# Performance work log

Hardware: AMD Instinct MI355X
Metric: run time of the kernel (lower is better)

Reference implementation:

```python
import jax, jax.numpy as jnp
import numpy as np

B, S, CC, CF, E, H, NH = 16, 1024, 8, 8, 64, 1024, 16
DH = H // NH
VOCAB = 10000
EPS = 1e-5


def layer_norm(x, g, b):
    m = x.mean(-1, keepdims=True)
    v = x.var(-1, keepdims=True)
    return (x - m) / jnp.sqrt(v + EPS) * g + b


def setup_inputs():
    key = jax.random.key(0)
    ks = jax.random.split(key, 30)
    f32 = jnp.float32
    n = lambda k, shp, s=0.02: jax.random.normal(k, shp, f32) * s
    inp = {}
    inp['cate_x'] = jax.random.randint(ks[0], (B, S, CC), 0, VOCAB)
    inp['cont_x'] = jax.random.normal(ks[1], (B, S, CF), f32)
    inp['mask'] = jax.random.randint(ks[2], (B, S), 0, 2)
    # parameters
    inp['emb_table'] = n(ks[3], (VOCAB, E)).at[0].set(0.0)  # padding_idx=0
    inp['cate_W'] = n(ks[4], (CC * E, H)); inp['cate_b'] = jnp.zeros((H,), f32)
    inp['cate_ln_g'] = jnp.ones((H,), f32); inp['cate_ln_b'] = jnp.zeros((H,), f32)
    inp['bn_g'] = jnp.ones((CF,), f32); inp['bn_b'] = jnp.zeros((CF,), f32)
    inp['cont_W'] = n(ks[5], (CF, H)); inp['cont_b'] = jnp.zeros((H,), f32)
    inp['cont_ln_g'] = jnp.ones((H,), f32); inp['cont_ln_b'] = jnp.zeros((H,), f32)
    inp['comb_W'] = n(ks[6], (2 * H, H)); inp['comb_b'] = jnp.zeros((H,), f32)
    inp['comb_ln_g'] = jnp.ones((H,), f32); inp['comb_ln_b'] = jnp.zeros((H,), f32)
    inp['Wq'] = n(ks[7], (H, H)); inp['bq'] = jnp.zeros((H,), f32)
    inp['Wk'] = n(ks[8], (H, H)); inp['bk'] = jnp.zeros((H,), f32)
    inp['Wv'] = n(ks[9], (H, H)); inp['bv'] = jnp.zeros((H,), f32)
    inp['Wo'] = n(ks[10], (H, H)); inp['bo'] = jnp.zeros((H,), f32)
    return inp


def reference(cate_x, cont_x, mask, emb_table, cate_W, cate_b, cate_ln_g, cate_ln_b,
              bn_g, bn_b, cont_W, cont_b, cont_ln_g, cont_ln_b,
              comb_W, comb_b, comb_ln_g, comb_ln_b,
              Wq, bq, Wk, bk, Wv, bv, Wo, bo):
    # categorical path: embed -> flatten cols -> Linear+LN
    cate_emb = emb_table[cate_x].reshape(B, S, CC * E)
    cate_h = layer_norm(cate_emb @ cate_W + cate_b, cate_ln_g, cate_ln_b)
    # continuous path: BatchNorm1d over flattened (B*S, CF) with batch stats
    xf = cont_x.reshape(-1, CF)
    mu = xf.mean(0)
    var = xf.var(0)  # biased, as torch BN normalization
    xn = ((xf - mu) / jnp.sqrt(var + EPS) * bn_g + bn_b).reshape(B, S, CF)
    cont_h = layer_norm(xn @ cont_W + cont_b, cont_ln_g, cont_ln_b)
    # combine: ReLU -> Linear -> LN
    seq = jax.nn.relu(jnp.concatenate([cate_h, cont_h], axis=2))
    x = layer_norm(seq @ comb_W + comb_b, comb_ln_g, comb_ln_b)  # [B,S,H]
    # multi-head attention (dropout is identity in eval)
    Q = (x @ Wq + bq).reshape(B, S, NH, DH)
    K = (x @ Wk + bk).reshape(B, S, NH, DH)
    V = (x @ Wv + bv).reshape(B, S, NH, DH)
    scores = jnp.einsum('bqhd,bkhd->bhqk', Q, K) / np.sqrt(DH).astype(np.float32)
    # faithful to source: mask broadcast over the QUERY axis
    scores = jnp.where(mask[:, None, :, None] == 0, -1e7, scores)
    attn = jax.nn.softmax(scores, axis=-1)
    out = jnp.einsum('bhqk,bkhd->bqhd', attn, V).reshape(B, S, H)
    out = out @ Wo + bo
    return out[:, -1:, -1]  # [B,1]
```

## Files before the change

### kernel.cpp

```cpp
#include <hip/hip_runtime.h>
#include <hip/hip_bf16.h>
#include <math.h>

#define EPS 1e-5f

typedef unsigned short u16;
typedef __attribute__((ext_vector_type(8))) short bf16x8;
typedef __attribute__((ext_vector_type(4))) float f32x4;

__device__ __forceinline__ float b2f(u16 u) {
  union { unsigned int i; float f; } v; v.i = ((unsigned int)u) << 16; return v.f;
}
__device__ __forceinline__ u16 f2b(float f) {
  union { float f; unsigned int i; } v; v.f = f;
  unsigned int r = v.i + 0x7fff + ((v.i >> 16) & 1);
  return (u16)(r >> 16);
}

__device__ __forceinline__ void gload_lds16(const u16* g, u16* l) {
  __builtin_amdgcn_global_load_lds(
      (const __attribute__((address_space(1))) unsigned int*)g,
      (__attribute__((address_space(3))) unsigned int*)l, 16, 0, 0);
}

__global__ __launch_bounds__(256) void prep_k(
    const float* __restrict__ cx, float* __restrict__ part_bn,
    float* __restrict__ outacc,
    const float* __restrict__ emb, u16* __restrict__ embb,
    const float* __restrict__ cate_W, u16* __restrict__ cateWT,
    const float* __restrict__ comb_W, u16* __restrict__ combWT,
    const float* __restrict__ Wv, const float* __restrict__ Wo,
    float* __restrict__ wvo) {
  __shared__ float shmem[64 * 65];
  const int bid = blockIdx.x, tid = threadIdx.x;

  if (bid == 0) {
    if (tid < 16) outacc[tid] = 0.f;
    return;
  }
  if (bid <= 64) {
    int pb = bid - 1;
    int gid = pb * 256 + tid;
    float4 a = ((const float4*)cx)[2 * gid];
    float4 b = ((const float4*)cx)[2 * gid + 1];
    float v[16];
    v[0] = a.x; v[1] = a.y; v[2] = a.z; v[3] = a.w;
    v[4] = b.x; v[5] = b.y; v[6] = b.z; v[7] = b.w;
#pragma unroll
    for (int i = 0; i < 8; ++i) v[8 + i] = v[i] * v[i];
#pragma unroll
    for (int off = 32; off; off >>= 1)
#pragma unroll
      for (int i = 0; i < 16; ++i) v[i] += __shfl_down(v[i], off);
    int l = tid & 63, wv_ = tid >> 6;
    if (l == 0)
#pragma unroll
      for (int i = 0; i < 16; ++i) shmem[wv_ * 16 + i] = v[i];
    __syncthreads();
    if (tid < 16)
      part_bn[pb * 16 + tid] = shmem[tid] + shmem[16 + tid] + shmem[32 + tid] + shmem[48 + tid];
    return;
  }
  if (bid <= 689) {
    int i = (bid - 65) * 256 + tid;
    if (i < 160000) {
      float4 v = ((const float4*)emb)[i];
      ushort4 u; u.x = f2b(v.x); u.y = f2b(v.y); u.z = f2b(v.z); u.w = f2b(v.w);
      ((ushort4*)embb)[i] = u;
    }
    return;
  }
  if (bid <= 1329) {
    const float* W; u16* WT; int K, local;
    if (bid <= 817) { W = cate_W; WT = cateWT; K = 512;  local = bid - 690; }
    else            { W = comb_W; WT = combWT; K = 2048; local = bid - 818; }
    int n0 = (local & 15) * 64, k0 = (local >> 4) * 64;
    int c = tid & 63, r0 = tid >> 6;
#pragma unroll
    for (int i = 0; i < 16; ++i) {
      int r = r0 + i * 4;
      shmem[r * 65 + c] = W[(size_t)(k0 + r) * 1024 + n0 + c];
    }
    __syncthreads();
#pragma unroll
    for (int i = 0; i < 16; ++i) {
      int r = r0 + i * 4;
      WT[(size_t)(n0 + r) * K + k0 + c] = f2b(shmem[c * 65 + r]);
    }
    return;
  }
  {
    int local = bid - 1330;
    int h = local >> 2, jc = local & 3;
    if (tid < 64) shmem[tid] = Wo[(size_t)(h * 64 + tid) * 1024 + 1023];
    __syncthreads();
    int j = jc * 256 + tid;
    const float* vr = Wv + (size_t)j * 1024 + h * 64;
    float s = 0.f;
    for (int d4 = 0; d4 < 64; d4 += 4) {
      float4 w4 = *(const float4*)(vr + d4);
      s = fmaf(w4.x, shmem[d4], s);
      s = fmaf(w4.y, shmem[d4 + 1], s);
      s = fmaf(w4.z, shmem[d4 + 2], s);
      s = fmaf(w4.w, shmem[d4 + 3], s);
    }
    wvo[h * 1024 + j] = s;
  }
}

template <int MODE, int VC>
__global__ __launch_bounds__(512) void gemm256(
    const u16* __restrict__ A0, const u16* __restrict__ A1,
    const int* __restrict__ idx, const u16* __restrict__ embb,
    const u16* __restrict__ BT, const float* __restrict__ bias,
    u16* __restrict__ C, int K) {
  __shared__ u16 As[2][2][8192];
  __shared__ u16 Bs[2][2][8192];
  const int tid = threadIdx.x;
  const int bid = blockIdx.x;
  const int chunk = gridDim.x >> 3;
  const int swz = (bid & 7) * chunk + (bid >> 3);
  const int row0 = (swz >> 2) * 256;
  const int col0 = (swz & 3) * 256;

  const int rr8 = tid >> 3;
  const int p8  = tid & 7;
  const int sl  = p8 ^ (rr8 & 7);

  const int l   = tid & 63;
  const int w   = tid >> 6;
  const int wrh = w >> 2;
  const int wcq = w & 3;
  const int hb  = wcq >> 1;
  const int rbb = (wcq & 1) * 64;
  const int lr  = l & 15;
  const int lk  = l >> 4;

  f32x4 acc[8][4];
#pragma unroll
  for (int m = 0; m < 8; ++m)
#pragma unroll
    for (int n = 0; n < 4; ++n) acc[m][n] = (f32x4){0.f, 0.f, 0.f, 0.f};

  const int nt = K >> 6;

  auto stage = [&](int t, int buf) {
    const int k0 = t << 6;
#pragma unroll
    for (int h = 0; h < 2; ++h)
#pragma unroll
      for (int i = 0; i < 2; ++i) {
        int ar = row0 + h * 128 + i * 64 + rr8;
        const u16* asrc;
        if (MODE == 1) {
          int id = idx[ar * 8 + (k0 >> 6)];
          asrc = embb + (size_t)id * 64 + sl * 8;
        } else {
          const u16* base = (k0 < 1024) ? A0 : A1;
          asrc = base + (size_t)ar * 1024 + (k0 & 1023) + sl * 8;
        }
        gload_lds16(asrc, &As[buf][h][i * 4096 + tid * 8]);
      }
#pragma unroll
    for (int h = 0; h < 2; ++h)
#pragma unroll
      for (int i = 0; i < 2; ++i) {
        int br = col0 + h * 128 + i * 64 + rr8;
        gload_lds16(BT + (size_t)br * K + k0 + sl * 8,
                    &Bs[buf][h][i * 4096 + tid * 8]);
      }
  };

  stage(0, 0);

  for (int t = 0; t < nt; ++t) {
    if (t + 1 < nt) {
      stage(t + 1, (t + 1) & 1);
      if (VC == 8) asm volatile("s_waitcnt vmcnt(8)" ::: "memory");
      else         asm volatile("s_waitcnt vmcnt(12)" ::: "memory");
    } else {
      asm volatile("s_waitcnt vmcnt(0)" ::: "memory");
    }
    __builtin_amdgcn_s_barrier();

    const int cur = t & 1;

    auto loadA = [&](bf16x8 (&af)[2][2], int q) {
#pragma unroll
      for (int mm = 0; mm < 2; ++mm)
#pragma unroll
        for (int ks = 0; ks < 2; ++ks) {
          int rowa = (q * 2 + mm) * 16 + lr;
          int ph = (ks * 4 + lk) ^ (lr & 7);
          af[mm][ks] = *(const bf16x8*)&As[cur][wrh][rowa * 64 + ph * 8];
        }
    };

    bf16x8 bfr[4][2];
#pragma unroll
    for (int n = 0; n < 4; ++n)
#pragma unroll
      for (int ks = 0; ks < 2; ++ks) {
        int rowb = rbb + n * 16 + lr;
        int ph = (ks * 4 + lk) ^ (lr & 7);
        bfr[n][ks] = *(const bf16x8*)&Bs[cur][hb][rowb * 64 + ph * 8];
      }

    auto mfma_quad = [&](bf16x8 (&af)[2][2], int q) {
      __builtin_amdgcn_s_setprio(1);
#pragma unroll
      for (int ks = 0; ks < 2; ++ks)
#pragma unroll
        for (int mm = 0; mm < 2; ++mm)
#pragma unroll
          for (int n = 0; n < 4; ++n)
            acc[q * 2 + mm][n] = __builtin_amdgcn_mfma_f32_16x16x32_bf16(
                af[mm][ks], bfr[n][ks], acc[q * 2 + mm][n], 0, 0, 0);
      __builtin_amdgcn_s_setprio(0);
    };

    bf16x8 afr0[2][2], afr1[2][2];
    loadA(afr0, 0);
    loadA(afr1, 1);
    mfma_quad(afr0, 0);
    loadA(afr0, 2);
    mfma_quad(afr1, 1);
    loadA(afr1, 3);
    mfma_quad(afr0, 2);
    mfma_quad(afr1, 3);

    if (t + 1 < nt) __builtin_amdgcn_s_barrier();
  }

  float bv_[4];
#pragma unroll
  for (int n = 0; n < 4; ++n) bv_[n] = bias[col0 + wcq * 64 + n * 16 + lr];
#pragma unroll
  for (int m = 0; m < 8; ++m) {
#pragma unroll
    for (int n = 0; n < 4; ++n) {
      int cc = col0 + wcq * 64 + n * 16 + lr;
#pragma unroll
      for (int q4 = 0; q4 < 4; ++q4) {
        int rr = row0 + wrh * 128 + m * 16 + lk * 4 + q4;
        C[(size_t)rr * 1024 + cc] = f2b(acc[m][n][q4] + bv_[n]);
      }
    }
  }
}

__global__ __launch_bounds__(256) void ln_k(u16* __restrict__ buf,
                                            const float* __restrict__ g,
                                            const float* __restrict__ b, int relu) {
  int lane = threadIdx.x & 63, wave = threadIdx.x >> 6;
  size_t row = (size_t)blockIdx.x * 4 + wave;
  u16* p = buf + row * 1024 + lane * 16;
  uint4 u0 = *(uint4*)p;
  uint4 u1 = *(uint4*)(p + 8);
  float x[16];
#pragma unroll
  for (int i = 0; i < 4; ++i) {
    unsigned int w0 = ((unsigned int*)&u0)[i];
    unsigned int w1 = ((unsigned int*)&u1)[i];
    x[2 * i]     = b2f((u16)(w0 & 0xffff));
    x[2 * i + 1] = b2f((u16)(w0 >> 16));
    x[8 + 2 * i]     = b2f((u16)(w1 & 0xffff));
    x[8 + 2 * i + 1] = b2f((u16)(w1 >> 16));
  }
  float s = 0.f, s2 = 0.f;
#pragma unroll
  for (int i = 0; i < 16; ++i) { s += x[i]; s2 += x[i] * x[i]; }
#pragma unroll
  for (int off = 32; off; off >>= 1) { s += __shfl_xor(s, off); s2 += __shfl_xor(s2, off); }
  float mean = s * (1.f / 1024.f);
  float var = s2 * (1.f / 1024.f) - mean * mean;
  float rs = rsqrtf(var + EPS);
  float y[16];
#pragma unroll
  for (int q = 0; q < 4; ++q) {
    float4 gv = *(const float4*)(g + lane * 16 + q * 4);
    float4 bv = *(const float4*)(b + lane * 16 + q * 4);
    y[4 * q]     = (x[4 * q]     - mean) * rs * gv.x + bv.x;
    y[4 * q + 1] = (x[4 * q + 1] - mean) * rs * gv.y + bv.y;
    y[4 * q + 2] = (x[4 * q + 2] - mean) * rs * gv.z + bv.z;
    y[4 * q + 3] = (x[4 * q + 3] - mean) * rs * gv.w + bv.w;
  }
  if (relu)
#pragma unroll
    for (int i = 0; i < 16; ++i) y[i] = fmaxf(y[i], 0.f);
  uint4 o0, o1;
#pragma unroll
  for (int i = 0; i < 4; ++i) {
    ((unsigned int*)&o0)[i] = (unsigned int)f2b(y[2 * i]) | ((unsigned int)f2b(y[2 * i + 1]) << 16);
    ((unsigned int*)&o1)[i] = (unsigned int)f2b(y[8 + 2 * i]) | ((unsigned int)f2b(y[8 + 2 * i + 1]) << 16);
  }
  *(uint4*)p = o0;
  *(uint4*)(p + 8) = o1;
}

__global__ __launch_bounds__(256) void cont_k(const float* __restrict__ cx,
                                              const float* __restrict__ part_bn,
                                              const float* __restrict__ bn_g,
                                              const float* __restrict__ bn_b,
                                              const float* __restrict__ W,
                                              const float* __restrict__ cb,
                                              const float* __restrict__ g,
                                              const float* __restrict__ bb,
                                              u16* __restrict__ out) {
  int row0 = blockIdx.x * 8, tid = threadIdx.x;
  __shared__ float sp[4][16];
  __shared__ float tt[16];
  __shared__ float ab[2][8];
  __shared__ float xn[8][8];
  __shared__ float rr1[4][8], rr2[4][8];

  if (tid < 64) {
    int f = tid & 15, qd = tid >> 4;
    float s = 0.f;
    for (int j = qd * 16; j < qd * 16 + 16; ++j) s += part_bn[j * 16 + f];
    sp[qd][f] = s;
  }
  __syncthreads();
  if (tid < 16) tt[tid] = sp[0][tid] + sp[1][tid] + sp[2][tid] + sp[3][tid];
  __syncthreads();
  if (tid < 8) {
    float mu = tt[tid] * (1.f / 16384.f);
    float var = tt[8 + tid] * (1.f / 16384.f) - mu * mu;
    float a = rsqrtf(var + EPS) * bn_g[tid];
    ab[0][tid] = a;
    ab[1][tid] = bn_b[tid] - mu * a;
  }
  __syncthreads();
  if (tid < 64) {
    int r = tid >> 3, f = tid & 7;
    xn[r][f] = ab[0][f] * cx[(row0 + r) * 8 + f] + ab[1][f];
  }
  __syncthreads();

  int c = tid * 4;
  float4 cbv = *(const float4*)(cb + c);
  float acc[8][4];
#pragma unroll
  for (int r = 0; r < 8; ++r) {
    acc[r][0] = cbv.x; acc[r][1] = cbv.y; acc[r][2] = cbv.z; acc[r][3] = cbv.w;
  }
  for (int k = 0; k < 8; ++k) {
    float4 w4 = *(const float4*)(W + k * 1024 + c);
#pragma unroll
    for (int r = 0; r < 8; ++r) {
      float xv = xn[r][k];
      acc[r][0] = fmaf(xv, w4.x, acc[r][0]);
      acc[r][1] = fmaf(xv, w4.y, acc[r][1]);
      acc[r][2] = fmaf(xv, w4.z, acc[r][2]);
      acc[r][3] = fmaf(xv, w4.w, acc[r][3]);
    }
  }
  float s1[8], s2[8];
#pragma unroll
  for (int r = 0; r < 8; ++r) {
    s1[r] = acc[r][0] + acc[r][1] + acc[r][2] + acc[r][3];
    s2[r] = acc[r][0] * acc[r][0] + acc[r][1] * acc[r][1] +
            acc[r][2] * acc[r][2] + acc[r][3] * acc[r][3];
  }
#pragma unroll
  for (int off = 32; off; off >>= 1)
#pragma unroll
    for (int r = 0; r < 8; ++r) {
      s1[r] += __shfl_down(s1[r], off);
      s2[r] += __shfl_down(s2[r], off);
    }
  int lane = tid & 63, wv = tid >> 6;
  if (lane == 0)
#pragma unroll
    for (int r = 0; r < 8; ++r) { rr1[wv][r] = s1[r]; rr2[wv][r] = s2[r]; }
  __syncthreads();
  float4 gv = *(const float4*)(g + c);
  float4 bv = *(const float4*)(bb + c);
#pragma unroll
  for (int r = 0; r < 8; ++r) {
    float ss = rr1[0][r] + rr1[1][r] + rr1[2][r] + rr1[3][r];
    float qq = rr2[0][r] + rr2[1][r] + rr2[2][r] + rr2[3][r];
    float mean = ss * (1.f / 1024.f);
    float var = qq * (1.f / 1024.f) - mean * mean;
    float rs = rsqrtf(var + EPS);
    float y0 = fmaxf((acc[r][0] - mean) * rs * gv.x + bv.x, 0.f);
    float y1 = fmaxf((acc[r][1] - mean) * rs * gv.y + bv.y, 0.f);
    float y2 = fmaxf((acc[r][2] - mean) * rs * gv.z + bv.z, 0.f);
    float y3 = fmaxf((acc[r][3] - mean) * rs * gv.w + bv.w, 0.f);
    ushort4 o; o.x = f2b(y0); o.y = f2b(y1); o.z = f2b(y2); o.w = f2b(y3);
    *(ushort4*)(out + (size_t)(row0 + r) * 1024 + c) = o;
  }
}

__global__ __launch_bounds__(256) void qproj_k(const u16* __restrict__ x,
                                               const float* __restrict__ Wq,
                                               const float* __restrict__ bq,
                                               float* __restrict__ q) {
  __shared__ u16 xs[16][1024];
  __shared__ float part[16][16][16];
  int tid = threadIdx.x;
  for (int i = tid; i < 4096; i += 256) {
    int b = i >> 8, off = (i & 255) * 4;
    *(ushort4*)&xs[b][off] =
        *(const ushort4*)(x + ((size_t)(b * 1024 + 1023)) * 1024 + off);
  }
  __syncthreads();
  int c = tid & 15;
  int col = blockIdx.x * 16 + c;
  int kq = tid >> 4;
  float acc[16];
#pragma unroll
  for (int b = 0; b < 16; ++b) acc[b] = 0.f;
  for (int k = kq * 64; k < kq * 64 + 64; ++k) {
    float wv = Wq[(size_t)k * 1024 + col];
#pragma unroll
    for (int b = 0; b < 16; ++b) acc[b] = fmaf(b2f(xs[b][k]), wv, acc[b]);
  }
#pragma unroll
  for (int b = 0; b < 16; ++b) part[kq][b][c] = acc[b];
  __syncthreads();
  if (tid < 256) {
    int b = tid >> 4, cc = tid & 15;
    float s = 0.f;
#pragma unroll
    for (int j = 0; j < 16; ++j) s += part[j][b][cc];
    q[b * 1024 + blockIdx.x * 16 + cc] = s + bq[blockIdx.x * 16 + cc];
  }
}

__global__ __launch_bounds__(256) void kq_k(const float* __restrict__ Wk,
                                            const float* __restrict__ bk,
                                            const float* __restrict__ q,
                                            u16* __restrict__ qtb,
                                            float* __restrict__ bkq) {
  int h = blockIdx.x >> 2, jc = blockIdx.x & 3;
  int tid = threadIdx.x;
  __shared__ float Qs[16][64];
  for (int i = tid; i < 1024; i += 256) {
    int b = i >> 6, d = i & 63;
    Qs[b][d] = q[b * 1024 + h * 64 + d];
  }
  __syncthreads();
  int j = jc * 256 + tid;
  float acc[16];
#pragma unroll
  for (int b = 0; b < 16; ++b) acc[b] = 0.f;
  const float* wr = Wk + (size_t)j * 1024 + h * 64;
  for (int d4 = 0; d4 < 64; d4 += 4) {
    float4 w4 = *(const float4*)(wr + d4);
#pragma unroll
    for (int b = 0; b < 16; ++b) {
      acc[b] = fmaf(w4.x, Qs[b][d4], acc[b]);
      acc[b] = fmaf(w4.y, Qs[b][d4 + 1], acc[b]);
      acc[b] = fmaf(w4.z, Qs[b][d4 + 2], acc[b]);
      acc[b] = fmaf(w4.w, Qs[b][d4 + 3], acc[b]);
    }
  }
#pragma unroll
  for (int b = 0; b < 16; ++b) qtb[((size_t)b * 16 + h) * 1024 + j] = f2b(acc[b]);
  if (jc == 0 && tid < 16) {
    int b = tid;
    float s = 0.f;
    for (int d = 0; d < 64; ++d) s = fmaf(bk[h * 64 + d], Qs[b][d], s);
    bkq[b * 16 + h] = s;
  }
}

__global__ __launch_bounds__(256) void score_k(const u16* __restrict__ x,
                                               const u16* __restrict__ qtb,
                                               const float* __restrict__ bkq,
                                               const int* __restrict__ mask,
                                               float* __restrict__ sc) {
  int b = blockIdx.x >> 4, kc = blockIdx.x & 15;
  int tid = threadIdx.x;
  int l = tid & 63, w = tid >> 6;
  int keybase = kc * 64 + w * 16;
  int lr = l & 15, ls = l >> 4;
  int masked = (mask[b * 1024 + 1023] == 0);

  f32x4 acc = (f32x4){0.f, 0.f, 0.f, 0.f};
  const u16* xb = x + (size_t)b * 1024 * 1024;
  const u16* qb = qtb + (size_t)b * 16 * 1024;
  for (int k0 = 0; k0 < 1024; k0 += 32) {
    bf16x8 bfr = *(const bf16x8*)&qb[(size_t)lr * 1024 + k0 + ls * 8];
    bf16x8 afr = *(const bf16x8*)&xb[(size_t)(keybase + lr) * 1024 + k0 + ls * 8];
    acc = __builtin_amdgcn_mfma_f32_16x16x32_bf16(afr, bfr, acc, 0, 0, 0);
  }
  int h = lr;
  float bq_ = bkq[b * 16 + h];
#pragma unroll
  for (int q = 0; q < 4; ++q) {
    int key = keybase + ls * 4 + q;
    float v = masked ? 0.f : (acc[q] + bq_) * 0.125f;
    sc[((size_t)b * 16 + h) * 1024 + key] = v;
  }
}

__global__ __launch_bounds__(256) void attnw_k(float* __restrict__ sc) {
  int bh = blockIdx.x, tid = threadIdx.x;
  float* row = sc + (size_t)bh * 1024;
  float4 v = ((float4*)row)[tid];
  float m = fmaxf(fmaxf(v.x, v.y), fmaxf(v.z, v.w));
#pragma unroll
  for (int off = 32; off; off >>= 1) m = fmaxf(m, __shfl_down(m, off));
  __shared__ float rm[4], rs_[4];
  int lane = tid & 63, wv = tid >> 6;
  if (lane == 0) rm[wv] = m;
  __syncthreads();
  m = fmaxf(fmaxf(rm[0], rm[1]), fmaxf(rm[2], rm[3]));
  float e0 = expf(v.x - m), e1 = expf(v.y - m), e2 = expf(v.z - m), e3 = expf(v.w - m);
  float s = e0 + e1 + e2 + e3;
#pragma unroll
  for (int off = 32; off; off >>= 1) s += __shfl_down(s, off);
  if (lane == 0) rs_[wv] = s;
  __syncthreads();
  s = rs_[0] + rs_[1] + rs_[2] + rs_[3];
  float inv = 1.f / s;
  float4 o; o.x = e0 * inv; o.y = e1 * inv; o.z = e2 * inv; o.w = e3 * inv;
  ((float4*)row)[tid] = o;
}

__global__ __launch_bounds__(256) void ctx_k(const float* __restrict__ p,
                                             const u16* __restrict__ x,
                                             const float* __restrict__ wvo,
                                             float* __restrict__ outacc) {
  int b = blockIdx.x >> 4, kc = blockIdx.x & 15;
  int tid = threadIdx.x;
  __shared__ float pl[64][16];
  for (int i = tid; i < 1024; i += 256) {
    int kk = i >> 4, hh = i & 15;
    pl[kk][hh] = p[((size_t)b * 16 + hh) * 1024 + kc * 64 + kk];
  }
  __syncthreads();
  float acc[16][4];
#pragma unroll
  for (int h = 0; h < 16; ++h)
#pragma unroll
    for (int j = 0; j < 4; ++j) acc[h][j] = 0.f;
  const u16* xb = x + ((size_t)(b * 1024 + kc * 64)) * 1024 + tid * 4;
  for (int k = 0; k < 64; ++k) {
    ushort4 u = *(const ushort4*)(xb + (size_t)k * 1024);
    float x0 = b2f(u.x), x1 = b2f(u.y), x2 = b2f(u.z), x3 = b2f(u.w);
#pragma unroll
    for (int h4 = 0; h4 < 4; ++h4) {
      float4 pv = *(const float4*)&pl[k][h4 * 4];
      acc[h4 * 4 + 0][0] = fmaf(pv.x, x0, acc[h4 * 4 + 0][0]);
      acc[h4 * 4 + 0][1] = fmaf(pv.x, x1, acc[h4 * 4 + 0][1]);
      acc[h4 * 4 + 0][2] = fmaf(pv.x, x2, acc[h4 * 4 + 0][2]);
      acc[h4 * 4 + 0][3] = fmaf(pv.x, x3, acc[h4 * 4 + 0][3]);
      acc[h4 * 4 + 1][0] = fmaf(pv.y, x0, acc[h4 * 4 + 1][0]);
      acc[h4 * 4 + 1][1] = fmaf(pv.y, x1, acc[h4 * 4 + 1][1]);
      acc[h4 * 4 + 1][2] = fmaf(pv.y, x2, acc[h4 * 4 + 1][2]);
      acc[h4 * 4 + 1][3] = fmaf(pv.y, x3, acc[h4 * 4 + 1][3]);
      acc[h4 * 4 + 2][0] = fmaf(pv.z, x0, acc[h4 * 4 + 2][0]);
      acc[h4 * 4 + 2][1] = fmaf(pv.z, x1, acc[h4 * 4 + 2][1]);
      acc[h4 * 4 + 2][2] = fmaf(pv.z, x2, acc[h4 * 4 + 2][2]);
      acc[h4 * 4 + 2][3] = fmaf(pv.z, x3, acc[h4 * 4 + 2][3]);
      acc[h4 * 4 + 3][0] = fmaf(pv.w, x0, acc[h4 * 4 + 3][0]);
      acc[h4 * 4 + 3][1] = fmaf(pv.w, x1, acc[h4 * 4 + 3][1]);
      acc[h4 * 4 + 3][2] = fmaf(pv.w, x2, acc[h4 * 4 + 3][2]);
      acc[h4 * 4 + 3][3] = fmaf(pv.w, x3, acc[h4 * 4 + 3][3]);
    }
  }
  float s = 0.f;
#pragma unroll
  for (int h = 0; h < 16; ++h) {
    float4 w4 = *(const float4*)&wvo[h * 1024 + tid * 4];
    s += acc[h][0] * w4.x + acc[h][1] * w4.y + acc[h][2] * w4.z + acc[h][3] * w4.w;
  }
#pragma unroll
  for (int off = 32; off; off >>= 1) s += __shfl_down(s, off);
  __shared__ float r[4];
  int lane = tid & 63, wv = tid >> 6;
  if (lane == 0) r[wv] = s;
  __syncthreads();
  if (tid == 0) atomicAdd(&outacc[b], r[0] + r[1] + r[2] + r[3]);
}

__global__ __launch_bounds__(256) void bfinal_k(const float* __restrict__ outacc,
                                                const float* __restrict__ bv,
                                                const float* __restrict__ Wo,
                                                const float* __restrict__ bo,
                                                float* __restrict__ out) {
  int tid = threadIdx.x;
  float s = 0.f;
  for (int i = tid; i < 1024; i += 256) s = fmaf(bv[i], Wo[(size_t)i * 1024 + 1023], s);
#pragma unroll
  for (int off = 32; off; off >>= 1) s += __shfl_down(s, off);
  __shared__ float r[4];
  int lane = tid & 63, wv = tid >> 6;
  if (lane == 0) r[wv] = s;
  __syncthreads();
  float bc = r[0] + r[1] + r[2] + r[3] + bo[1023];
  if (tid < 16) out[tid] = outacc[tid] + bc;
}

extern "C" void kernel_launch(void* const* d_in, const int* in_sizes, int n_in,
                              void* d_out, int out_size, void* d_ws, size_t ws_size,
                              hipStream_t stream) {
  const int*   cate_x  = (const int*)d_in[0];
  const float* cont_x  = (const float*)d_in[1];
  const int*   mask    = (const int*)d_in[2];
  const float* emb     = (const float*)d_in[3];
  const float* cate_W  = (const float*)d_in[4];
  const float* cate_b  = (const float*)d_in[5];
  const float* cate_g  = (const float*)d_in[6];
  const float* cate_bb = (const float*)d_in[7];
  const float* bn_g    = (const float*)d_in[8];
  const float* bn_b    = (const float*)d_in[9];
  const float* cont_W  = (const float*)d_in[10];
  const float* cont_b  = (const float*)d_in[11];
  const float* cont_g  = (const float*)d_in[12];
  const float* cont_bb = (const float*)d_in[13];
  const float* Wq = (const float*)d_in[18]; const float* bq = (const float*)d_in[19];
  const float* Wk = (const float*)d_in[20]; const float* bk = (const float*)d_in[21];
  const float* Wv = (const float*)d_in[22]; const float* bv = (const float*)d_in[23];
  const float* Wo = (const float*)d_in[24]; const float* bo = (const float*)d_in[25];
  const float* comb_W  = (const float*)d_in[14];
  const float* comb_b  = (const float*)d_in[15];
  const float* comb_g  = (const float*)d_in[16];
  const float* comb_bb = (const float*)d_in[17];
  float* out = (float*)d_out;

  char* w = (char*)d_ws;
  float* stats   = (float*)w;
  float* outacc  = stats + 16;
  float* part_bn = (float*)(w + 256);
  float* qbuf    = (float*)(w + 8192);
  u16* embb      = (u16*)(w + 131328);
  u16* cateWT    = (u16*)(w + 1411328);
  u16* combWT    = (u16*)(w + 2459904);
  float* sc      = (float*)(w + 6654208);
  u16*   qtb     = (u16*)(w + 7702784);
  float* wvo     = (float*)(w + 8227072);
  float* bkq     = (float*)(w + 8292608);
  u16* X1        = (u16*)(w + 10848512);
  u16* X2        = X1 + (size_t)16777216;
  u16* xb        = X2 + (size_t)16777216;

  prep_k<<<1394, 256, 0, stream>>>(cont_x, part_bn, outacc, emb, embb,
                                   cate_W, cateWT, comb_W, combWT, Wv, Wo, wvo);

  gemm256<1, 12><<<256, 512, 0, stream>>>(nullptr, nullptr, cate_x, embb, cateWT,
                                          cate_b, X1, 512);
  ln_k<<<4096, 256, 0, stream>>>(X1, cate_g, cate_bb, 1);
  cont_k<<<2048, 256, 0, stream>>>(cont_x, part_bn, bn_g, bn_b, cont_W, cont_b,
                                   cont_g, cont_bb, X2);
  gemm256<2, 8><<<256, 512, 0, stream>>>(X1, X2, nullptr, nullptr, combWT,
                                         comb_b, xb, 2048);
  ln_k<<<4096, 256, 0, stream>>>(xb, comb_g, comb_bb, 0);

  qproj_k<<<64, 256, 0, stream>>>(xb, Wq, bq, qbuf);
  kq_k<<<64, 256, 0, stream>>>(Wk, bk, qbuf, qtb, bkq);
  score_k<<<256, 256, 0, stream>>>(xb, qtb, bkq, mask, sc);
  attnw_k<<<256, 256, 0, stream>>>(sc);
  ctx_k<<<256, 256, 0, stream>>>(sc, xb, wvo, outacc);
  bfinal_k<<<1, 256, 0, stream>>>(outacc, bv, Wo, bo, out);
}
```

Before: 212.5 us.

## Interleave half-tile global-to-LDS staging with MFMA quads in 256x256 GEMM

Restructures the bf16 GEMM main loop into a two-tile unrolled schedule. Global-to-LDS loads for the next A tile and the B tile after it are issued in halves between individual MFMA quads, with extra barriers and lgkmcnt waits around each step. The goal is finer-grained overlap of memory traffic with matrix math, in the style of a ping-pong schedule. In exchange it adds many more barriers per K step, relies on hand-counted vmcnt values, and assumes nt is even.

```diff
diff --git a/kernel.cpp b/kernel.cpp
--- a/kernel.cpp
+++ b/kernel.cpp
@@ -108,7 +108,7 @@
   }
 }
 
-template <int MODE, int VC>
+template <int MODE>
 __global__ __launch_bounds__(512) void gemm256(
     const u16* __restrict__ A0, const u16* __restrict__ A1,
     const int* __restrict__ idx, const u16* __restrict__ embb,
@@ -143,93 +143,135 @@
     for (int n = 0; n < 4; ++n) acc[m][n] = (f32x4){0.f, 0.f, 0.f, 0.f};
 
   const int nt = K >> 6;
-
-  auto stage = [&](int t, int buf) {
+  const int nit = nt >> 1;
+
+  auto stageA = [&](int t, int h) {
     const int k0 = t << 6;
-#pragma unroll
-    for (int h = 0; h < 2; ++h)
-#pragma unroll
-      for (int i = 0; i < 2; ++i) {
-        int ar = row0 + h * 128 + i * 64 + rr8;
-        const u16* asrc;
-        if (MODE == 1) {
-          int id = idx[ar * 8 + (k0 >> 6)];
-          asrc = embb + (size_t)id * 64 + sl * 8;
-        } else {
-          const u16* base = (k0 < 1024) ? A0 : A1;
-          asrc = base + (size_t)ar * 1024 + (k0 & 1023) + sl * 8;
-        }
-        gload_lds16(asrc, &As[buf][h][i * 4096 + tid * 8]);
+    const int buf = t & 1;
+#pragma unroll
+    for (int i = 0; i < 2; ++i) {
+      int ar = row0 + h * 128 + i * 64 + rr8;
+      const u16* asrc;
+      if (MODE == 1) {
+        int id = idx[ar * 8 + (k0 >> 6)];
+        asrc = embb + (size_t)id * 64 + sl * 8;
+      } else {
+        const u16* base = (k0 < 1024) ? A0 : A1;
+        asrc = base + (size_t)ar * 1024 + (k0 & 1023) + sl * 8;
       }
-#pragma unroll
-    for (int h = 0; h < 2; ++h)
-#pragma unroll
-      for (int i = 0; i < 2; ++i) {
-        int br = col0 + h * 128 + i * 64 + rr8;
-        gload_lds16(BT + (size_t)br * K + k0 + sl * 8,
-                    &Bs[buf][h][i * 4096 + tid * 8]);
-      }
+      gload_lds16(asrc, &As[buf][h][i * 4096 + tid * 8]);
+    }
   };
-
-  stage(0, 0);
-
-  for (int t = 0; t < nt; ++t) {
-    if (t + 1 < nt) {
-      stage(t + 1, (t + 1) & 1);
-      if (VC == 8) asm volatile("s_waitcnt vmcnt(8)" ::: "memory");
-      else         asm volatile("s_waitcnt vmcnt(12)" ::: "memory");
-    } else {
-      asm volatile("s_waitcnt vmcnt(0)" ::: "memory");
-    }
-    __builtin_amdgcn_s_barrier();
-
-    const int cur = t & 1;
-
-    auto loadA = [&](bf16x8 (&af)[2][2], int q) {
-#pragma unroll
-      for (int mm = 0; mm < 2; ++mm)
-#pragma unroll
-        for (int ks = 0; ks < 2; ++ks) {
-          int rowa = (q * 2 + mm) * 16 + lr;
-          int ph = (ks * 4 + lk) ^ (lr & 7);
-          af[mm][ks] = *(const bf16x8*)&As[cur][wrh][rowa * 64 + ph * 8];
-        }
-    };
-
-    bf16x8 bfr[4][2];
+  auto stageB = [&](int t, int h) {
+    const int k0 = t << 6;
+    const int buf = t & 1;
+#pragma unroll
+    for (int i = 0; i < 2; ++i) {
+      int br = col0 + h * 128 + i * 64 + rr8;
+      gload_lds16(BT + (size_t)br * K + k0 + sl * 8,
+                  &Bs[buf][h][i * 4096 + tid * 8]);
+    }
+  };
+
+  bf16x8 bfr[4][2];
+  auto loadB = [&](int buf) {
 #pragma unroll
     for (int n = 0; n < 4; ++n)
 #pragma unroll
       for (int ks = 0; ks < 2; ++ks) {
         int rowb = rbb + n * 16 + lr;
         int ph = (ks * 4 + lk) ^ (lr & 7);
-        bfr[n][ks] = *(const bf16x8*)&Bs[cur][hb][rowb * 64 + ph * 8];
+        bfr[n][ks] = *(const bf16x8*)&Bs[buf][hb][rowb * 64 + ph * 8];
       }
-
-    auto mfma_quad = [&](bf16x8 (&af)[2][2], int q) {
-      __builtin_amdgcn_s_setprio(1);
-#pragma unroll
-      for (int ks = 0; ks < 2; ++ks)
-#pragma unroll
-        for (int mm = 0; mm < 2; ++mm)
-#pragma unroll
-          for (int n = 0; n < 4; ++n)
-            acc[q * 2 + mm][n] = __builtin_amdgcn_mfma_f32_16x16x32_bf16(
-                af[mm][ks], bfr[n][ks], acc[q * 2 + mm][n], 0, 0, 0);
-      __builtin_amdgcn_s_setprio(0);
-    };
-
-    bf16x8 afr0[2][2], afr1[2][2];
-    loadA(afr0, 0);
-    loadA(afr1, 1);
-    mfma_quad(afr0, 0);
-    loadA(afr0, 2);
-    mfma_quad(afr1, 1);
-    loadA(afr1, 3);
-    mfma_quad(afr0, 2);
-    mfma_quad(afr1, 3);
-
-    if (t + 1 < nt) __builtin_amdgcn_s_barrier();
+  };
+  auto loadA = [&](bf16x8 (&af)[2][2], int buf, int q) {
+#pragma unroll
+    for (int mm = 0; mm < 2; ++mm)
+#pragma unroll
+      for (int ks = 0; ks < 2; ++ks) {
+        int rowa = (q * 2 + mm) * 16 + lr;
+        int ph = (ks * 4 + lk) ^ (lr & 7);
+        af[mm][ks] = *(const bf16x8*)&As[buf][wrh][rowa * 64 + ph * 8];
+      }
+  };
+  auto mfma_quad = [&](bf16x8 (&af)[2][2], int q) {
+    __builtin_amdgcn_s_setprio(1);
+#pragma unroll
+    for (int ks = 0; ks < 2; ++ks)
+#pragma unroll
+      for (int mm = 0; mm < 2; ++mm)
+#pragma unroll
+        for (int n = 0; n < 4; ++n)
+          acc[q * 2 + mm][n] = __builtin_amdgcn_mfma_f32_16x16x32_bf16(
+              af[mm][ks], bfr[n][ks], acc[q * 2 + mm][n], 0, 0, 0);
+    __builtin_amdgcn_s_setprio(0);
+  };
+
+  stageA(0, 0); stageA(0, 1);
+  stageB(0, 0); stageB(0, 1);
+  stageB(1, 0); stageB(1, 1);
+  asm volatile("s_waitcnt vmcnt(4)" ::: "memory");
+  __builtin_amdgcn_s_barrier();
+
+  for (int it = 0; it < nit; ++it) {
+    const int T = it * 2;
+    const bool more = (T + 2 < nt);
+    bf16x8 af[2][2];
+
+    loadB(0); loadA(af, 0, 0);
+    stageA(T + 1, 0);
+    __builtin_amdgcn_s_barrier();
+    asm volatile("s_waitcnt lgkmcnt(0)" ::: "memory");
+    mfma_quad(af, 0);
+    __builtin_amdgcn_s_barrier();
+    loadA(af, 0, 1);
+    stageA(T + 1, 1);
+    __builtin_amdgcn_s_barrier();
+    asm volatile("s_waitcnt lgkmcnt(0)" ::: "memory");
+    mfma_quad(af, 1);
+    __builtin_amdgcn_s_barrier();
+    loadA(af, 0, 2);
+    if (more) stageB(T + 2, 0);
+    __builtin_amdgcn_s_barrier();
+    asm volatile("s_waitcnt lgkmcnt(0)" ::: "memory");
+    mfma_quad(af, 2);
+    __builtin_amdgcn_s_barrier();
+    loadA(af, 0, 3);
+    if (more) stageB(T + 2, 1);
+    __builtin_amdgcn_s_barrier();
+    asm volatile("s_waitcnt lgkmcnt(0)" ::: "memory");
+    mfma_quad(af, 3);
+    if (more) asm volatile("s_waitcnt vmcnt(4)" ::: "memory");
+    else      asm volatile("s_waitcnt vmcnt(0)" ::: "memory");
+    __builtin_amdgcn_s_barrier();
+
+    loadB(1); loadA(af, 1, 0);
+    if (more) stageA(T + 2, 0);
+    __builtin_amdgcn_s_barrier();
+    asm volatile("s_waitcnt lgkmcnt(0)" ::: "memory");
+    mfma_quad(af, 0);
+    __builtin_amdgcn_s_barrier();
+    loadA(af, 1, 1);
+    if (more) stageA(T + 2, 1);
+    __builtin_amdgcn_s_barrier();
+    asm volatile("s_waitcnt lgkmcnt(0)" ::: "memory");
+    mfma_quad(af, 1);
+    __builtin_amdgcn_s_barrier();
+    loadA(af, 1, 2);
+    if (more) stageB(T + 3, 0);
+    __builtin_amdgcn_s_barrier();
+    asm volatile("s_waitcnt lgkmcnt(0)" ::: "memory");
+    mfma_quad(af, 2);
+    __builtin_amdgcn_s_barrier();
+    loadA(af, 1, 3);
+    if (more) stageB(T + 3, 1);
+    __builtin_amdgcn_s_barrier();
+    asm volatile("s_waitcnt lgkmcnt(0)" ::: "memory");
+    mfma_quad(af, 3);
+    if (it + 1 < nit) {
+      asm volatile("s_waitcnt vmcnt(4)" ::: "memory");
+      __builtin_amdgcn_s_barrier();
+    }
   }
 
   float bv_[4];
@@ -641,13 +683,13 @@
   prep_k<<<1394, 256, 0, stream>>>(cont_x, part_bn, outacc, emb, embb,
                                    cate_W, cateWT, comb_W, combWT, Wv, Wo, wvo);
 
-  gemm256<1, 12><<<256, 512, 0, stream>>>(nullptr, nullptr, cate_x, embb, cateWT,
-                                          cate_b, X1, 512);
+  gemm256<1><<<256, 512, 0, stream>>>(nullptr, nullptr, cate_x, embb, cateWT,
+                                      cate_b, X1, 512);
   ln_k<<<4096, 256, 0, stream>>>(X1, cate_g, cate_bb, 1);
   cont_k<<<2048, 256, 0, stream>>>(cont_x, part_bn, bn_g, bn_b, cont_W, cont_b,
                                    cont_g, cont_bb, X2);
-  gemm256<2, 8><<<256, 512, 0, stream>>>(X1, X2, nullptr, nullptr, combWT,
-                                         comb_b, xb, 2048);
+  gemm256<2><<<256, 512, 0, stream>>>(X1, X2, nullptr, nullptr, combWT,
+                                      comb_b, xb, 2048);
   ln_k<<<4096, 256, 0, stream>>>(xb, comb_g, comb_bb, 0);
 
   qproj_k<<<64, 256, 0, stream>>>(xb, Wq, bq, qbuf);
```

Result: no change. 210.1 us (-1.1%).
